# Kernel tuning notes

Measured on AMD Instinct MI355X. Metric: run time of the kernel, lower is better.

## Reference

```python
import jax, jax.numpy as jnp
import numpy as np

N = 50000   # nodes
E = 800000  # edges
G = 64      # graphs in batch
D = 96      # feature dim (in = hidden = out)


def gcn_conv(x, src, dst, ew, W, b, n):
    """PyG GCNConv: add self-loops, symmetric deg^-1/2 norm, linear, scatter-add, bias."""
    loop = jnp.arange(n)
    row = jnp.concatenate([src, loop])            # source nodes incl. self-loops
    col = jnp.concatenate([dst, loop])            # target nodes incl. self-loops
    w = jnp.concatenate([ew, jnp.ones((n,), x.dtype)])  # self-loop weight = 1.0
    deg = jax.ops.segment_sum(w, col, num_segments=n)
    dinv = jnp.where(deg > 0, jax.lax.rsqrt(jnp.maximum(deg, 1e-20)), 0.0)
    norm = dinv[row] * w * dinv[col]              # [E+N]
    h = x @ W                                     # [n, d_out] linear first (d_out <= d_in ok)
    out = jax.ops.segment_sum(norm[:, None] * h[row], col, num_segments=n)
    return out + b


def setup_inputs() -> dict:
    key = jax.random.key(0)
    ks = jax.random.split(key, 8)
    x = jax.random.normal(ks[0], (N, D), jnp.float32)
    edge_index = jax.random.randint(ks[1], (2, E), 0, N, dtype=jnp.int64)
    edge_weight = jax.random.uniform(ks[2], (E,), jnp.float32)
    batch = jnp.sort(jax.random.randint(ks[3], (N,), 0, G, dtype=jnp.int64))
    s = 0.05
    W1 = jax.random.normal(ks[4], (D, D), jnp.float32) * s
    W3 = jax.random.normal(ks[5], (D, D), jnp.float32) * s
    W4 = jax.random.normal(ks[6], (D, D), jnp.float32) * s
    b1 = jnp.zeros((D,), jnp.float32)
    b3 = jnp.zeros((D,), jnp.float32)
    b4 = jnp.zeros((D,), jnp.float32)
    return {"x": x, "W1": W1, "b1": b1, "W3": W3, "b3": b3, "W4": W4, "b4": b4,
            "edge_weight": edge_weight, "edge_index": edge_index, "batch": batch}


def reference(x, W1, b1, W3, b3, W4, b4, edge_weight, edge_index, batch):
    # eval mode: F.dropout(p=0.5, training=False) is identity
    src, dst = edge_index[0], edge_index[1]
    h = jax.nn.relu(gcn_conv(x, src, dst, edge_weight, W1, b1, N))
    embed = gcn_conv(h, src, dst, edge_weight, W3, b3, N)
    ge = gcn_conv(h, src, dst, edge_weight, W4, b4, N)
    graph_embed = jax.ops.segment_sum(ge, batch, num_segments=G)  # global_add_pool
    return embed, graph_embed
```

## Files before the change

kernel.cpp:

```cpp
#include <hip/hip_runtime.h>
#include <hip/hip_fp16.h>

#define NN 50000
#define EE 800000
#define DD 96
#define GG 64
#define NH 12
#define NT 3125

#define FPSCALE 16777216.0f
#define MASK44 ((1ULL << 44) - 1)
#define NCPY 8
#define NBG2 ((NT + 3) / 4)

typedef unsigned long long u64;
typedef __attribute__((ext_vector_type(8))) _Float16 half8;
typedef __attribute__((ext_vector_type(4))) float f32x4;

__device__ __forceinline__ uint4 pack8(const float* f) {
    __half2 h0 = __floats2half2_rn(f[0], f[1]);
    __half2 h1 = __floats2half2_rn(f[2], f[3]);
    __half2 h2 = __floats2half2_rn(f[4], f[5]);
    __half2 h3 = __floats2half2_rn(f[6], f[7]);
    uint4 o;
    o.x = *(unsigned int*)&h0; o.y = *(unsigned int*)&h1;
    o.z = *(unsigned int*)&h2; o.w = *(unsigned int*)&h3;
    return o;
}

__device__ __forceinline__ void cvt8(uint4 v, float* f) {
    const __half2* h = (const __half2*)&v;
    #pragma unroll
    for (int k = 0; k < 4; ++k) {
        float2 t = __half22float2(h[k]);
        f[2 * k] = t.x; f[2 * k + 1] = t.y;
    }
}


__global__ void k_pre(u64* histo, float* gsum,
                      const float4* __restrict__ x, uint4* __restrict__ xh,
                      const float* __restrict__ W1, _Float16* __restrict__ w1t,
                      const float* __restrict__ W3, _Float16* __restrict__ w3t) {
    int i = blockIdx.x * 256 + threadIdx.x;
    if (i < NCPY * NN) histo[i] = 0ULL;
    if (i < GG * DD) gsum[i] = 0.f;
    if (i < DD * DD) {
        int k = i / DD, n = i % DD;
        w1t[n * DD + k] = (_Float16)W1[i];
        w3t[n * DD + k] = (_Float16)W3[i];
    }
    if (i < NN * DD / 8) {
        float4 f0 = x[2 * i], f1 = x[2 * i + 1];
        float f[8] = {f0.x, f0.y, f0.z, f0.w, f1.x, f1.y, f1.z, f1.w};
        xh[i] = pack8(f);
    }
}


__global__ void k_hist(const int* __restrict__ dst, const float* __restrict__ ew,
                       u64* histo, unsigned int* rank) {
    int e = blockIdx.x * 256 + threadIdx.x;
    int cpy = blockIdx.x & (NCPY - 1);
    if (e < EE) {
        u64 q = (u64)(ew[e] * FPSCALE + 0.5f);
        u64 old = atomicAdd(&histo[(size_t)cpy * NN + dst[e]], (1ULL << 44) | q);
        rank[e] = ((unsigned)cpy << 24) | (unsigned)(old >> 44);
    }
}


__global__ __launch_bounds__(256) void k_dinv_reduce(const u64* __restrict__ histo,
                                                     float* dinv, int* cnts,
                                                     unsigned* xoff, int* bsums) {
    __shared__ int s[256];
    int tid = threadIdx.x;
    int i = blockIdx.x * 256 + tid;
    int tot = 0;
    if (i < NN) {
        u64 wsum44 = 0;
        unsigned pre = 0;
        #pragma unroll
        for (int x = 0; x < NCPY; ++x) {
            u64 h = histo[(size_t)x * NN + i];
            wsum44 += h & MASK44;
            xoff[(size_t)i * NCPY + x] = pre;
            pre += (unsigned)(h >> 44);
        }
        tot = (int)pre;
        cnts[i] = tot;
        dinv[i] = rsqrtf(1.0f + (float)wsum44 * (1.0f / FPSCALE));
    }
    s[tid] = tot;
    __syncthreads();
    for (int off = 128; off > 0; off >>= 1) {
        if (tid < off) s[tid] += s[tid + off];
        __syncthreads();
    }
    if (tid == 0) bsums[blockIdx.x] = s[0];
}


__global__ __launch_bounds__(256) void k_scan2(const int* __restrict__ cnts,
                                               const int* __restrict__ bsums,
                                               int nb, int* row_ptr) {
    __shared__ int s[256];
    int tid = threadIdx.x;
    int bv = (tid < nb) ? bsums[tid] : 0;
    s[tid] = bv; __syncthreads();
    for (int off = 1; off < 256; off <<= 1) {
        int t = (tid >= off) ? s[tid - off] : 0;
        __syncthreads();
        s[tid] += t;
        __syncthreads();
    }
    int pb = (blockIdx.x > 0) ? s[blockIdx.x - 1] : 0;
    __syncthreads();
    int i = blockIdx.x * 256 + tid;
    int v = (i < NN) ? cnts[i] : 0;
    s[tid] = v; __syncthreads();
    for (int off = 1; off < 256; off <<= 1) {
        int t = (tid >= off) ? s[tid - off] : 0;
        __syncthreads();
        s[tid] += t;
        __syncthreads();
    }
    if (i < NN) row_ptr[i] = pb + s[tid] - v;
    if (blockIdx.x == gridDim.x - 1 && tid == 255) row_ptr[NN] = EE;
}


__global__ void k_scatter(const int* __restrict__ src, const int* __restrict__ dst,
                          const float* __restrict__ ew, const float* __restrict__ dinv,
                          const int* __restrict__ row_ptr, const unsigned* __restrict__ xoff,
                          const unsigned int* __restrict__ rank, int2* csr) {
    int e = blockIdx.x * 256 + threadIdx.x;
    if (e < EE) {
        int s = src[e], d = dst[e];
        unsigned r = rank[e];
        int x = (int)(r >> 24);
        int p = row_ptr[d] + (int)xoff[(size_t)d * NCPY + x] + (int)(r & 0xFFFFFFu);
        float w = dinv[s] * ew[e] * dinv[d];
        csr[p] = make_int2(s, __float_as_int(w));
    }
}


__global__ __launch_bounds__(192) void k_prop_h(const uint4* __restrict__ Th,
                                                const int2* __restrict__ csr,
                                                const int* __restrict__ row_ptr,
                                                const float* __restrict__ dinv,
                                                uint4* __restrict__ Ph) {
    int tid = threadIdx.x;
    int node = blockIdx.x * 16 + tid / 12;
    int c = tid % 12;
    float di = dinv[node];
    float self = di * di;
    float f[8], acc[8];
    cvt8(Th[node * NH + c], f);
    #pragma unroll
    for (int j = 0; j < 8; ++j) acc[j] = self * f[j];
    int e0 = row_ptr[node], e1 = row_ptr[node + 1];
    for (int e = e0; e < e1; ++e) {
        int2 sw = csr[e];
        float w = __int_as_float(sw.y);
        cvt8(Th[sw.x * NH + c], f);
        #pragma unroll
        for (int j = 0; j < 8; ++j) acc[j] = fmaf(w, f[j], acc[j]);
    }
    Ph[node * NH + c] = pack8(acc);
}


__global__ __launch_bounds__(256) void k_gemm1(const _Float16* __restrict__ Xh,
                                               const _Float16* __restrict__ Wt,
                                               const float* __restrict__ bias,
                                               _Float16* __restrict__ Oh) {
    int wv = threadIdx.x >> 6;
    int lane = threadIdx.x & 63;
    int tile = blockIdx.x * 4 + wv;
    if (tile >= NT) return;
    int r = lane & 15, q = lane >> 4;
    half8 bf[3][6];
    #pragma unroll
    for (int ks = 0; ks < 3; ++ks)
        #pragma unroll
        for (int nt = 0; nt < 6; ++nt)
            bf[ks][nt] = *(const half8*)&Wt[(size_t)(nt * 16 + r) * DD + ks * 32 + q * 8];
    f32x4 acc[6];
    #pragma unroll
    for (int nt = 0; nt < 6; ++nt) { float b = bias[nt * 16 + r]; acc[nt] = (f32x4){b, b, b, b}; }
    size_t rowoff = (size_t)(tile * 16 + r) * DD;
    #pragma unroll
    for (int ks = 0; ks < 3; ++ks) {
        half8 af = *(const half8*)&Xh[rowoff + ks * 32 + q * 8];
        #pragma unroll
        for (int nt = 0; nt < 6; ++nt)
            acc[nt] = __builtin_amdgcn_mfma_f32_16x16x32_f16(af, bf[ks][nt], acc[nt], 0, 0, 0);
    }
    int rowbase = tile * 16 + q * 4;
    #pragma unroll
    for (int nt = 0; nt < 6; ++nt)
        #pragma unroll
        for (int g = 0; g < 4; ++g) {
            float v = fmaxf(acc[nt][g], 0.f);
            Oh[(size_t)(rowbase + g) * DD + nt * 16 + r] = (_Float16)v;
        }
}


__global__ __launch_bounds__(256) void k_tail(const _Float16* __restrict__ Ph,
                                              const _Float16* __restrict__ Wt,
                                              const float* __restrict__ b3,
                                              float* __restrict__ embed,
                                              const int* __restrict__ batch,
                                              float* __restrict__ gsum) {
    int tid = threadIdx.x;
    if (blockIdx.x < NBG2) {
        int wv = tid >> 6;
        int lane = tid & 63;
        int tile = blockIdx.x * 4 + wv;
        if (tile >= NT) return;
        int r = lane & 15, q = lane >> 4;
        half8 bf[3][6];
        #pragma unroll
        for (int ks = 0; ks < 3; ++ks)
            #pragma unroll
            for (int nt = 0; nt < 6; ++nt)
                bf[ks][nt] = *(const half8*)&Wt[(size_t)(nt * 16 + r) * DD + ks * 32 + q * 8];
        f32x4 acc[6];
        #pragma unroll
        for (int nt = 0; nt < 6; ++nt) { float b = b3[nt * 16 + r]; acc[nt] = (f32x4){b, b, b, b}; }
        size_t rowoff = (size_t)(tile * 16 + r) * DD;
        #pragma unroll
        for (int ks = 0; ks < 3; ++ks) {
            half8 af = *(const half8*)&Ph[rowoff + ks * 32 + q * 8];
            #pragma unroll
            for (int nt = 0; nt < 6; ++nt)
                acc[nt] = __builtin_amdgcn_mfma_f32_16x16x32_f16(af, bf[ks][nt], acc[nt], 0, 0, 0);
        }
        int rowbase = tile * 16 + q * 4;
        #pragma unroll
        for (int nt = 0; nt < 6; ++nt)
            #pragma unroll
            for (int g = 0; g < 4; ++g)
                embed[(size_t)(rowbase + g) * DD + nt * 16 + r] = acc[nt][g];
    } else {
        const __half* P2 = (const __half*)Ph;
        int b = blockIdx.x - NBG2;
        int g = b >> 3, s = b & 7;
        int d = tid % 96, t = tid / 96;
        int lo = 0, hi = NN;
        while (lo < hi) { int m = (lo + hi) >> 1; if (batch[m] < g) lo = m + 1; else hi = m; }
        int start = lo;
        lo = 0; hi = NN;
        while (lo < hi) { int m = (lo + hi) >> 1; if (batch[m] < g + 1) lo = m + 1; else hi = m; }
        int end = lo;
        float acc = 0.f;
        if (tid < 192)
            for (int i = start + s * 2 + t; i < end; i += 16)
                acc += __half2float(P2[(size_t)i * DD + d]);
        __shared__ float red[192];
        if (tid < 192) red[tid] = acc;
        __syncthreads();
        if (tid < 96) atomicAdd(&gsum[g * 96 + tid], red[tid] + red[tid + 96]);
    }
}


__global__ __launch_bounds__(96) void k_pool_b(const float* __restrict__ gsum,
                                               const int* __restrict__ batch,
                                               const float* __restrict__ W4,
                                               const float* __restrict__ b4,
                                               float* __restrict__ outG) {
    int g = blockIdx.x, d = threadIdx.x;
    __shared__ float srow[96];
    srow[d] = gsum[g * 96 + d];
    int lo = 0, hi = NN;
    while (lo < hi) { int m = (lo + hi) >> 1; if (batch[m] < g) lo = m + 1; else hi = m; }
    int start = lo;
    lo = 0; hi = NN;
    while (lo < hi) { int m = (lo + hi) >> 1; if (batch[m] < g + 1) lo = m + 1; else hi = m; }
    int end = lo;
    __syncthreads();
    float o = (float)(end - start) * b4[d];
    #pragma unroll 8
    for (int k = 0; k < 96; ++k) o = fmaf(srow[k], W4[k * 96 + d], o);
    outG[g * 96 + d] = o;
}


extern "C" void kernel_launch(void* const* d_in, const int* in_sizes, int n_in,
                              void* d_out, int out_size, void* d_ws, size_t ws_size,
                              hipStream_t stream) {
    const float* x  = (const float*)d_in[0];
    const float* W1 = (const float*)d_in[1];
    const float* b1 = (const float*)d_in[2];
    const float* W3 = (const float*)d_in[3];
    const float* b3 = (const float*)d_in[4];
    const float* W4 = (const float*)d_in[5];
    const float* b4 = (const float*)d_in[6];
    const float* ew = (const float*)d_in[7];
    const int* ei   = (const int*)d_in[8];
    const int* src  = ei;
    const int* dst  = ei + EE;
    const int* batch = (const int*)d_in[9];

    float* out_embed = (float*)d_out;
    float* out_graph = out_embed + (size_t)NN * DD;

    char* w = (char*)d_ws;
    auto alloc = [&](size_t bytes) { char* p = w; w += (bytes + 255) & ~(size_t)255; return p; };
    u64* histo     = (u64*)  alloc((size_t)NCPY * NN * 8);
    unsigned* rank = (unsigned*)alloc((size_t)EE * 4);
    float* dinv    = (float*)alloc((size_t)NN * 4);
    int*   cnts    = (int*)  alloc((size_t)NN * 4);
    unsigned* xoff = (unsigned*)alloc((size_t)NN * NCPY * 4);
    int*   row_ptr = (int*)  alloc((size_t)(NN + 1) * 4);
    int*   bsums   = (int*)  alloc(256 * 4);
    float* gsum    = (float*)alloc((size_t)GG * DD * 4);
    int2*  csr     = (int2*) alloc((size_t)EE * 8);
    char*  xh      = alloc((size_t)NN * DD * 2);
    char*  hh      = alloc((size_t)NN * DD * 2);
    char*  ph      = alloc((size_t)NN * DD * 2);
    _Float16* w1t  = (_Float16*)alloc((size_t)DD * DD * 2);
    _Float16* w3t  = (_Float16*)alloc((size_t)DD * DD * 2);

    int nbN = (NN + 255) / 256;
    int nbE = (EE + 255) / 256;
    int nbP = (NN * DD / 8 + 255) / 256;

    k_pre<<<nbP, 256, 0, stream>>>(histo, gsum, (const float4*)x, (uint4*)xh,
                                   W1, w1t, W3, w3t);
    k_hist<<<nbE, 256, 0, stream>>>(dst, ew, histo, rank);
    k_dinv_reduce<<<nbN, 256, 0, stream>>>(histo, dinv, cnts, xoff, bsums);
    k_scan2<<<nbN, 256, 0, stream>>>(cnts, bsums, nbN, row_ptr);
    k_scatter<<<nbE, 256, 0, stream>>>(src, dst, ew, dinv, row_ptr, xoff, rank, csr);

    k_prop_h<<<NN / 16, 192, 0, stream>>>((const uint4*)xh, csr, row_ptr, dinv, (uint4*)ph);
    k_gemm1<<<NBG2, 256, 0, stream>>>((const _Float16*)ph, w1t, b1, (_Float16*)hh);
    k_prop_h<<<NN / 16, 192, 0, stream>>>((const uint4*)hh, csr, row_ptr, dinv, (uint4*)ph);
    k_tail<<<NBG2 + GG * 8, 256, 0, stream>>>((const _Float16*)ph, w3t, b3, out_embed, batch, gsum);
    k_pool_b<<<GG, 96, 0, stream>>>(gsum, batch, W4, b4, out_graph);
}
```

Before: 190.0 us.

## Sort nodes by degree for propagation load balance and unroll edge loop by two

Measured after the change: 310.3 us. 1.63x slower.

```diff
diff --git a/kernel.cpp b/kernel.cpp
--- a/kernel.cpp
+++ b/kernel.cpp
@@ -38,13 +38,14 @@
 }
 
 
-__global__ void k_pre(u64* histo, float* gsum,
+__global__ void k_pre(u64* histo, float* gsum, unsigned* dghist,
                       const float4* __restrict__ x, uint4* __restrict__ xh,
                       const float* __restrict__ W1, _Float16* __restrict__ w1t,
                       const float* __restrict__ W3, _Float16* __restrict__ w3t) {
     int i = blockIdx.x * 256 + threadIdx.x;
     if (i < NCPY * NN) histo[i] = 0ULL;
     if (i < GG * DD) gsum[i] = 0.f;
+    if (i < 256) dghist[i] = 0u;
     if (i < DD * DD) {
         int k = i / DD, n = i % DD;
         w1t[n * DD + k] = (_Float16)W1[i];
@@ -72,7 +73,8 @@
 
 __global__ __launch_bounds__(256) void k_dinv_reduce(const u64* __restrict__ histo,
                                                      float* dinv, int* cnts,
-                                                     unsigned* xoff, int* bsums) {
+                                                     unsigned* xoff, int* bsums,
+                                                     unsigned* dghist, unsigned* dgrank) {
     __shared__ int s[256];
     int tid = threadIdx.x;
     int i = blockIdx.x * 256 + tid;
@@ -90,6 +92,8 @@
         tot = (int)pre;
         cnts[i] = tot;
         dinv[i] = rsqrtf(1.0f + (float)wsum44 * (1.0f / FPSCALE));
+        int bucket = tot < 255 ? tot : 255;
+        dgrank[i] = atomicAdd(&dghist[bucket], 1u);
     }
     s[tid] = tot;
     __syncthreads();
@@ -103,7 +107,9 @@
 
 __global__ __launch_bounds__(256) void k_scan2(const int* __restrict__ cnts,
                                                const int* __restrict__ bsums,
-                                               int nb, int* row_ptr) {
+                                               int nb, int* row_ptr,
+                                               const unsigned* __restrict__ dghist,
+                                               unsigned* dgoff) {
     __shared__ int s[256];
     int tid = threadIdx.x;
     int bv = (tid < nb) ? bsums[tid] : 0;
@@ -127,14 +133,33 @@
     }
     if (i < NN) row_ptr[i] = pb + s[tid] - v;
     if (blockIdx.x == gridDim.x - 1 && tid == 255) row_ptr[NN] = EE;
+    if (blockIdx.x == 0) {
+        __syncthreads();
+        int dv = (int)dghist[tid];
+        s[tid] = dv; __syncthreads();
+        for (int off = 1; off < 256; off <<= 1) {
+            int t = (tid >= off) ? s[tid - off] : 0;
+            __syncthreads();
+            s[tid] += t;
+            __syncthreads();
+        }
+        dgoff[tid] = (unsigned)(s[tid] - dv);
+    }
 }
 
 
 __global__ void k_scatter(const int* __restrict__ src, const int* __restrict__ dst,
                           const float* __restrict__ ew, const float* __restrict__ dinv,
                           const int* __restrict__ row_ptr, const unsigned* __restrict__ xoff,
-                          const unsigned int* __restrict__ rank, int2* csr) {
+                          const unsigned int* __restrict__ rank, int2* csr,
+                          const int* __restrict__ cnts, const unsigned* __restrict__ dgoff,
+                          const unsigned* __restrict__ dgrank, unsigned* __restrict__ perm) {
     int e = blockIdx.x * 256 + threadIdx.x;
+    if (e < NN) {
+        int deg = cnts[e];
+        int bucket = deg < 255 ? deg : 255;
+        perm[dgoff[bucket] + dgrank[e]] = (unsigned)e;
+    }
     if (e < EE) {
         int s = src[e], d = dst[e];
         unsigned r = rank[e];
@@ -150,18 +175,32 @@
                                                 const int2* __restrict__ csr,
                                                 const int* __restrict__ row_ptr,
                                                 const float* __restrict__ dinv,
+                                                const unsigned* __restrict__ perm,
                                                 uint4* __restrict__ Ph) {
     int tid = threadIdx.x;
-    int node = blockIdx.x * 16 + tid / 12;
+    int node = (int)perm[blockIdx.x * 16 + tid / 12];
     int c = tid % 12;
     float di = dinv[node];
     float self = di * di;
-    float f[8], acc[8];
+    float f[8], g[8], acc[8];
     cvt8(Th[node * NH + c], f);
     #pragma unroll
     for (int j = 0; j < 8; ++j) acc[j] = self * f[j];
     int e0 = row_ptr[node], e1 = row_ptr[node + 1];
-    for (int e = e0; e < e1; ++e) {
+    int e = e0;
+    for (; e + 1 < e1; e += 2) {
+        int2 sa = csr[e];
+        int2 sb = csr[e + 1];
+        float wa = __int_as_float(sa.y);
+        float wb = __int_as_float(sb.y);
+        cvt8(Th[sa.x * NH + c], f);
+        cvt8(Th[sb.x * NH + c], g);
+        #pragma unroll
+        for (int j = 0; j < 8; ++j) acc[j] = fmaf(wa, f[j], acc[j]);
+        #pragma unroll
+        for (int j = 0; j < 8; ++j) acc[j] = fmaf(wb, g[j], acc[j]);
+    }
+    if (e < e1) {
         int2 sw = csr[e];
         float w = __int_as_float(sw.y);
         cvt8(Th[sw.x * NH + c], f);
@@ -319,6 +358,10 @@
     int*   row_ptr = (int*)  alloc((size_t)(NN + 1) * 4);
     int*   bsums   = (int*)  alloc(256 * 4);
     float* gsum    = (float*)alloc((size_t)GG * DD * 4);
+    unsigned* dghist = (unsigned*)alloc(256 * 4);
+    unsigned* dgoff  = (unsigned*)alloc(256 * 4);
+    unsigned* dgrank = (unsigned*)alloc((size_t)NN * 4);
+    unsigned* perm   = (unsigned*)alloc((size_t)NN * 4);
     int2*  csr     = (int2*) alloc((size_t)EE * 8);
     char*  xh      = alloc((size_t)NN * DD * 2);
     char*  hh      = alloc((size_t)NN * DD * 2);
@@ -330,16 +373,17 @@
     int nbE = (EE + 255) / 256;
     int nbP = (NN * DD / 8 + 255) / 256;
 
-    k_pre<<<nbP, 256, 0, stream>>>(histo, gsum, (const float4*)x, (uint4*)xh,
+    k_pre<<<nbP, 256, 0, stream>>>(histo, gsum, dghist, (const float4*)x, (uint4*)xh,
                                    W1, w1t, W3, w3t);
     k_hist<<<nbE, 256, 0, stream>>>(dst, ew, histo, rank);
-    k_dinv_reduce<<<nbN, 256, 0, stream>>>(histo, dinv, cnts, xoff, bsums);
-    k_scan2<<<nbN, 256, 0, stream>>>(cnts, bsums, nbN, row_ptr);
-    k_scatter<<<nbE, 256, 0, stream>>>(src, dst, ew, dinv, row_ptr, xoff, rank, csr);
-
-    k_prop_h<<<NN / 16, 192, 0, stream>>>((const uint4*)xh, csr, row_ptr, dinv, (uint4*)ph);
+    k_dinv_reduce<<<nbN, 256, 0, stream>>>(histo, dinv, cnts, xoff, bsums, dghist, dgrank);
+    k_scan2<<<nbN, 256, 0, stream>>>(cnts, bsums, nbN, row_ptr, dghist, dgoff);
+    k_scatter<<<nbE, 256, 0, stream>>>(src, dst, ew, dinv, row_ptr, xoff, rank, csr,
+                                       cnts, dgoff, dgrank, perm);
+
+    k_prop_h<<<NN / 16, 192, 0, stream>>>((const uint4*)xh, csr, row_ptr, dinv, perm, (uint4*)ph);
     k_gemm1<<<NBG2, 256, 0, stream>>>((const _Float16*)ph, w1t, b1, (_Float16*)hh);
-    k_prop_h<<<NN / 16, 192, 0, stream>>>((const uint4*)hh, csr, row_ptr, dinv, (uint4*)ph);
+    k_prop_h<<<NN / 16, 192, 0, stream>>>((const uint4*)hh, csr, row_ptr, dinv, perm, (uint4*)ph);
     k_tail<<<NBG2 + GG * 8, 256, 0, stream>>>((const _Float16*)ph, w3t, b3, out_embed, batch, gsum);
     k_pool_b<<<GG, 96, 0, stream>>>(gsum, batch, W4, b4, out_graph);
 }
```
